# Kernel tuning notes

Measured on AMD Instinct MI355X. Metric: run time of the kernel, lower is better.

The kernel has to match this reference:

```python
import jax, jax.numpy as jnp
import numpy as np

N = 8192
F_IN = 256
F_OUT = 64
NEG_SLOPE = 0.01


def setup_inputs() -> dict:
    key = jax.random.key(0)
    k1, k2, k3, k4 = jax.random.split(key, 4)
    h = jax.random.normal(k1, (N, F_IN), dtype=jnp.float32)
    adj = jax.random.randint(k2, (N, N), 0, 2).astype(jnp.float32)
    # xavier_uniform-scaled params
    W = jax.random.uniform(k3, (F_IN, F_OUT), jnp.float32, -1.0, 1.0) * np.sqrt(6.0 / (F_IN + F_OUT)).astype(np.float32)
    a = jax.random.uniform(k4, (2 * F_OUT, 1), jnp.float32, -1.0, 1.0) * np.sqrt(6.0 / (2 * F_OUT + 1)).astype(np.float32)
    return {"h": h, "adj": adj, "W": W, "a": a, "rel": 0}


def reference(h, adj, W, a, rel):
    # Wh: [N, F']
    Wh = h @ W
    # Decompose additive score: e_ij = LeakyReLU(a1.Wh_i + a2.Wh_j)
    # (equivalent to cat([Wh_i, Wh_j]) @ a, without the [N,N,2F'] tensor)
    a1 = a[:F_OUT, 0]
    a2 = a[F_OUT:, 0]
    f1 = Wh @ a1  # [N]
    f2 = Wh @ a2  # [N]
    e = jax.nn.leaky_relu(f1[:, None] + f2[None, :], NEG_SLOPE)  # [N, N]
    e = jnp.where(adj > 0, e, -jnp.inf)
    attention = jax.nn.softmax(e, axis=1)  # dropout is identity at eval time
    h_prime = attention @ Wh  # [N, F']
    return h_prime, attention
```

## Files before the change

### kernel.cpp

```cpp
#include <hip/hip_runtime.h>
#include <hip/hip_bf16.h>

#define N 8192
#define FIN 256
#define FOUT 64
#define NEG_SLOPE 0.01f
#define CHUNK 256
#define NCHUNK (N / CHUNK)
#define ROWS_B 8

typedef float f32x4 __attribute__((ext_vector_type(4)));
typedef __bf16 bf16x8 __attribute__((ext_vector_type(8)));
typedef unsigned long long ull;

__device__ __forceinline__ float lk(float x) { return x >= 0.f ? x : NEG_SLOPE * x; }

__global__ __launch_bounds__(256) void gat_k1(const float* __restrict__ h,
                                              const float* __restrict__ W,
                                              const float* __restrict__ a,
                                              unsigned short* __restrict__ WhB,
                                              float* __restrict__ f1,
                                              float* __restrict__ f2) {
  __shared__ float Ws[FIN * FOUT];
  const int t = threadIdx.x;
  const int lane = t & 63;
  const int w = t >> 6;
  const size_t row0 = (size_t)blockIdx.x * 16;

  for (int i = t; i < FIN * FOUT / 4; i += 256)
    ((f32x4*)Ws)[i] = ((const f32x4*)W)[i];
  __syncthreads();

  const float* h0 = h + row0 * FIN;
  float acc[4] = {0.f, 0.f, 0.f, 0.f};
  #pragma unroll 4
  for (int c4 = 0; c4 < FIN; c4 += 4) {
    const f32x4 hv0 = *(const f32x4*)(h0 + (w + 0)  * FIN + c4);
    const f32x4 hv1 = *(const f32x4*)(h0 + (w + 4)  * FIN + c4);
    const f32x4 hv2 = *(const f32x4*)(h0 + (w + 8)  * FIN + c4);
    const f32x4 hv3 = *(const f32x4*)(h0 + (w + 12) * FIN + c4);
    #pragma unroll
    for (int j = 0; j < 4; ++j) {
      const float wv = Ws[(c4 + j) * FOUT + lane];
      acc[0] = fmaf(hv0[j], wv, acc[0]);
      acc[1] = fmaf(hv1[j], wv, acc[1]);
      acc[2] = fmaf(hv2[j], wv, acc[2]);
      acc[3] = fmaf(hv3[j], wv, acc[3]);
    }
  }

  const float a1k = a[lane];
  const float a2k = a[FOUT + lane];
  #pragma unroll
  for (int i = 0; i < 4; ++i) {
    const size_t row = row0 + (w + 4 * i);
    WhB[(((row >> 3) * 64) + lane) * 8 + (row & 7)] =
        __builtin_bit_cast(unsigned short, __float2bfloat16(acc[i]));
    float p1 = acc[i] * a1k, p2 = acc[i] * a2k;
    #pragma unroll
    for (int off = 32; off; off >>= 1) {
      p1 += __shfl_down(p1, off);
      p2 += __shfl_down(p2, off);
    }
    if (lane == 0) { f1[row] = p1; f2[row] = p2; }
  }
}

__global__ __launch_bounds__(512) void gat_k2a(const float* __restrict__ adj,
                                               const float* __restrict__ f1g,
                                               const float* __restrict__ f2g,
                                               ull* __restrict__ mskg,
                                               float* __restrict__ izg) {
  __shared__ float f2s[N];
  const int t = threadIdx.x;
  const int lane = t & 63;
  const int w = t >> 6;
  for (int i = t; i < N / 4; i += 512)
    ((f32x4*)f2s)[i] = ((const f32x4*)f2g)[i];
  __syncthreads();

  const int row = blockIdx.x * 8 + w;
  const float f1r = f1g[row];
  const f32x4* arow = (const f32x4*)(adj + (size_t)row * N);
  ull* mrow = mskg + (size_t)row * (NCHUNK * 4);

  float s = 0.f;
  #pragma unroll 8
  for (int c = 0; c < NCHUNK; ++c) {
    const f32x4 v = arow[c * 64 + lane];
    const f32x4 f = *(const f32x4*)&f2s[c * CHUNK + lane * 4];
    const ull b0 = __ballot(v.x > 0.f);
    const ull b1 = __ballot(v.y > 0.f);
    const ull b2 = __ballot(v.z > 0.f);
    const ull b3 = __ballot(v.w > 0.f);
    const ull bb = lane == 0 ? b0 : lane == 1 ? b1 : lane == 2 ? b2 : b3;
    if (lane < 4) mrow[c * 4 + lane] = bb;
    s += (v.x > 0.f) ? __expf(lk(f1r + f.x)) : 0.f;
    s += (v.y > 0.f) ? __expf(lk(f1r + f.y)) : 0.f;
    s += (v.z > 0.f) ? __expf(lk(f1r + f.z)) : 0.f;
    s += (v.w > 0.f) ? __expf(lk(f1r + f.w)) : 0.f;
  }
  #pragma unroll
  for (int off = 32; off; off >>= 1) s += __shfl_xor(s, off);
  if (lane == 0) izg[row] = 1.f / s;
}

__global__ __launch_bounds__(512) void gat_k2b(const ull* __restrict__ mskg,
                                               const float* __restrict__ f1g,
                                               const float* __restrict__ f2g,
                                               const float* __restrict__ izg,
                                               const unsigned short* __restrict__ WhB,
                                               float* __restrict__ att,
                                               float* __restrict__ hp) {
  __shared__ ull msk[ROWS_B * NCHUNK * 4];
  __shared__ __align__(16) unsigned char attb[16 * CHUNK * 2];
  __shared__ float red[4][64][4];
  __shared__ float f1s[ROWS_B], izs[ROWS_B];

  const int t = threadIdx.x;
  const int lane = t & 63;
  const int w = t >> 6;
  const size_t row0 = (size_t)blockIdx.x * ROWS_B;

  for (int i = t; i < ROWS_B * NCHUNK * 4; i += 512)
    msk[i] = mskg[row0 * (NCHUNK * 4) + i];
  for (int i = t; i < 16 * CHUNK * 2 / 4; i += 512)
    ((unsigned int*)attb)[i] = 0u;
  if (t < ROWS_B) { f1s[t] = f1g[row0 + t]; izs[t] = izg[row0 + t]; }
  __syncthreads();

  const int ks = w >> 2, nt = w & 3;
  const int r = w;
  const float f1r = f1s[r], z = izs[r];
  f32x4 acc = {0.f, 0.f, 0.f, 0.f};

  for (int c = 0; c < NCHUNK; ++c) {
    const f32x4 f = *(const f32x4*)&f2g[c * CHUNK + lane * 4];
    const ull b0 = msk[r * (NCHUNK * 4) + c * 4 + 0];
    const ull b1 = msk[r * (NCHUNK * 4) + c * 4 + 1];
    const ull b2 = msk[r * (NCHUNK * 4) + c * 4 + 2];
    const ull b3 = msk[r * (NCHUNK * 4) + c * 4 + 3];
    f32x4 p;
    p.x = ((b0 >> lane) & 1ull) ? __expf(lk(f1r + f.x)) * z : 0.f;
    p.y = ((b1 >> lane) & 1ull) ? __expf(lk(f1r + f.y)) * z : 0.f;
    p.z = ((b2 >> lane) & 1ull) ? __expf(lk(f1r + f.z)) * z : 0.f;
    p.w = ((b3 >> lane) & 1ull) ? __expf(lk(f1r + f.w)) * z : 0.f;
    __builtin_nontemporal_store(p, (f32x4*)(att + (row0 + r) * (size_t)N + c * CHUNK + lane * 4));
    const ull pk =
        (ull)__builtin_bit_cast(unsigned short, __float2bfloat16(p.x)) |
        ((ull)__builtin_bit_cast(unsigned short, __float2bfloat16(p.y)) << 16) |
        ((ull)__builtin_bit_cast(unsigned short, __float2bfloat16(p.z)) << 32) |
        ((ull)__builtin_bit_cast(unsigned short, __float2bfloat16(p.w)) << 48);
    int byte = r * (CHUNK * 2) + lane * 8;
    byte ^= (r & 7) << 4;
    *(ull*)(attb + byte) = pk;
    __syncthreads();

    #pragma unroll
    for (int s = 0; s < 4; ++s) {
      const int mf = ks * 4 + s;
      const int arow_ = lane & 15;
      int ab = arow_ * (CHUNK * 2) + mf * 64 + (lane >> 4) * 16;
      ab ^= (arow_ & 7) << 4;
      const bf16x8 afrag = *(const bf16x8*)(attb + ab);
      const int kg = c * 32 + mf * 4 + (lane >> 4);
      const bf16x8 bfrag = *(const bf16x8*)(WhB + ((size_t)kg * 64 + nt * 16 + (lane & 15)) * 8);
      acc = __builtin_amdgcn_mfma_f32_16x16x32_bf16(afrag, bfrag, acc, 0, 0, 0);
    }
    __syncthreads();
  }

  if (ks == 1) *(f32x4*)&red[nt][lane][0] = acc;
  __syncthreads();
  if (ks == 0) {
    const f32x4 o = acc + *(const f32x4*)&red[nt][lane][0];
    const int col = nt * 16 + (lane & 15);
    const int rbase = (lane >> 4) * 4;
    if (rbase < ROWS_B) {
      #pragma unroll
      for (int q = 0; q < 4; ++q)
        hp[(row0 + rbase + q) * FOUT + col] = o[q];
    }
  }
}

extern "C" void kernel_launch(void* const* d_in, const int* in_sizes, int n_in,
                              void* d_out, int out_size, void* d_ws, size_t ws_size,
                              hipStream_t stream) {
  const float* h   = (const float*)d_in[0];
  const float* adj = (const float*)d_in[1];
  const float* W   = (const float*)d_in[2];
  const float* a   = (const float*)d_in[3];

  float* hp  = (float*)d_out;
  float* att = hp + (size_t)N * FOUT;

  unsigned short* WhB = (unsigned short*)d_ws;
  float* f1 = (float*)((char*)d_ws + (size_t)N * FOUT * 2);
  float* f2 = f1 + N;
  float* iz = f2 + N;
  ull*   msk = (ull*)(iz + N);

  gat_k1 <<<N / 16, 256, 0, stream>>>(h, W, a, WhB, f1, f2);
  gat_k2a<<<N / 8, 512, 0, stream>>>(adj, f1, f2, msk, iz);
  gat_k2b<<<N / ROWS_B, 512, 0, stream>>>(msk, f1, f2, iz, WhB, att, hp);
}
```

Measured before the change: 534.5 us.

## Widen attention-matmul tile to 32 rows with double-buffered LDS and no split-K

The second-pass kernel now handles 32 rows per block instead of 8. Each wave computes four rows of attention and a full 16x16 MFMA output tile over the whole K chunk, so the split-K reduction and the wasted half-empty MFMA rows go away. The LDS attention buffer is double-buffered, which removes one barrier per chunk. Mask bits are read straight from global memory instead of being staged in LDS. The first-pass kernel also stops staging f2 in LDS and uses nontemporal loads for adj. The risk is fewer blocks (256) with fewer waves to hide latency, plus more global mask loads per wave.

```diff
diff --git a/kernel.cpp b/kernel.cpp
--- a/kernel.cpp
+++ b/kernel.cpp
@@ -7,7 +7,8 @@
 #define NEG_SLOPE 0.01f
 #define CHUNK 256
 #define NCHUNK (N / CHUNK)
-#define ROWS_B 8
+#define RB 32
+#define MWORDS (NCHUNK * 4)
 
 typedef float f32x4 __attribute__((ext_vector_type(4)));
 typedef __bf16 bf16x8 __attribute__((ext_vector_type(8)));
@@ -71,24 +72,19 @@
                                                const float* __restrict__ f2g,
                                                ull* __restrict__ mskg,
                                                float* __restrict__ izg) {
-  __shared__ float f2s[N];
   const int t = threadIdx.x;
   const int lane = t & 63;
   const int w = t >> 6;
-  for (int i = t; i < N / 4; i += 512)
-    ((f32x4*)f2s)[i] = ((const f32x4*)f2g)[i];
-  __syncthreads();
-
   const int row = blockIdx.x * 8 + w;
   const float f1r = f1g[row];
   const f32x4* arow = (const f32x4*)(adj + (size_t)row * N);
-  ull* mrow = mskg + (size_t)row * (NCHUNK * 4);
+  ull* mrow = mskg + (size_t)row * MWORDS;
 
   float s = 0.f;
-  #pragma unroll 8
+  #pragma unroll 4
   for (int c = 0; c < NCHUNK; ++c) {
-    const f32x4 v = arow[c * 64 + lane];
-    const f32x4 f = *(const f32x4*)&f2s[c * CHUNK + lane * 4];
+    const f32x4 v = __builtin_nontemporal_load(arow + c * 64 + lane);
+    const f32x4 f = *(const f32x4*)&f2g[c * CHUNK + lane * 4];
     const ull b0 = __ballot(v.x > 0.f);
     const ull b1 = __ballot(v.y > 0.f);
     const ull b2 = __ballot(v.z > 0.f);
@@ -112,76 +108,64 @@
                                                const unsigned short* __restrict__ WhB,
                                                float* __restrict__ att,
                                                float* __restrict__ hp) {
-  __shared__ ull msk[ROWS_B * NCHUNK * 4];
-  __shared__ __align__(16) unsigned char attb[16 * CHUNK * 2];
-  __shared__ float red[4][64][4];
-  __shared__ float f1s[ROWS_B], izs[ROWS_B];
-
+  __shared__ __align__(16) unsigned char attb[2][RB * CHUNK * 2];
   const int t = threadIdx.x;
   const int lane = t & 63;
   const int w = t >> 6;
-  const size_t row0 = (size_t)blockIdx.x * ROWS_B;
+  const int mt = w >> 2, nt = w & 3;
+  const size_t row0 = (size_t)blockIdx.x * RB;
 
-  for (int i = t; i < ROWS_B * NCHUNK * 4; i += 512)
-    msk[i] = mskg[row0 * (NCHUNK * 4) + i];
-  for (int i = t; i < 16 * CHUNK * 2 / 4; i += 512)
-    ((unsigned int*)attb)[i] = 0u;
-  if (t < ROWS_B) { f1s[t] = f1g[row0 + t]; izs[t] = izg[row0 + t]; }
-  __syncthreads();
+  float f1r_[4], z_[4];
+  #pragma unroll
+  for (int rr = 0; rr < 4; ++rr) {
+    f1r_[rr] = f1g[row0 + 4 * w + rr];
+    z_[rr]   = izg[row0 + 4 * w + rr];
+  }
 
-  const int ks = w >> 2, nt = w & 3;
-  const int r = w;
-  const float f1r = f1s[r], z = izs[r];
   f32x4 acc = {0.f, 0.f, 0.f, 0.f};
 
+  #pragma unroll 2
   for (int c = 0; c < NCHUNK; ++c) {
+    unsigned char* ab = attb[c & 1];
     const f32x4 f = *(const f32x4*)&f2g[c * CHUNK + lane * 4];
-    const ull b0 = msk[r * (NCHUNK * 4) + c * 4 + 0];
-    const ull b1 = msk[r * (NCHUNK * 4) + c * 4 + 1];
-    const ull b2 = msk[r * (NCHUNK * 4) + c * 4 + 2];
-    const ull b3 = msk[r * (NCHUNK * 4) + c * 4 + 3];
-    f32x4 p;
-    p.x = ((b0 >> lane) & 1ull) ? __expf(lk(f1r + f.x)) * z : 0.f;
-    p.y = ((b1 >> lane) & 1ull) ? __expf(lk(f1r + f.y)) * z : 0.f;
-    p.z = ((b2 >> lane) & 1ull) ? __expf(lk(f1r + f.z)) * z : 0.f;
-    p.w = ((b3 >> lane) & 1ull) ? __expf(lk(f1r + f.w)) * z : 0.f;
-    __builtin_nontemporal_store(p, (f32x4*)(att + (row0 + r) * (size_t)N + c * CHUNK + lane * 4));
-    const ull pk =
-        (ull)__builtin_bit_cast(unsigned short, __float2bfloat16(p.x)) |
-        ((ull)__builtin_bit_cast(unsigned short, __float2bfloat16(p.y)) << 16) |
-        ((ull)__builtin_bit_cast(unsigned short, __float2bfloat16(p.z)) << 32) |
-        ((ull)__builtin_bit_cast(unsigned short, __float2bfloat16(p.w)) << 48);
-    int byte = r * (CHUNK * 2) + lane * 8;
-    byte ^= (r & 7) << 4;
-    *(ull*)(attb + byte) = pk;
+    #pragma unroll
+    for (int rr = 0; rr < 4; ++rr) {
+      const int r = 4 * w + rr;
+      const ull* mrow = mskg + (row0 + r) * (size_t)MWORDS + c * 4;
+      const ull b0 = mrow[0], b1 = mrow[1], b2 = mrow[2], b3 = mrow[3];
+      f32x4 p;
+      p.x = ((b0 >> lane) & 1ull) ? __expf(lk(f1r_[rr] + f.x)) * z_[rr] : 0.f;
+      p.y = ((b1 >> lane) & 1ull) ? __expf(lk(f1r_[rr] + f.y)) * z_[rr] : 0.f;
+      p.z = ((b2 >> lane) & 1ull) ? __expf(lk(f1r_[rr] + f.z)) * z_[rr] : 0.f;
+      p.w = ((b3 >> lane) & 1ull) ? __expf(lk(f1r_[rr] + f.w)) * z_[rr] : 0.f;
+      __builtin_nontemporal_store(p, (f32x4*)(att + (row0 + r) * (size_t)N + c * CHUNK + lane * 4));
+      const ull pk =
+          (ull)__builtin_bit_cast(unsigned short, __float2bfloat16(p.x)) |
+          ((ull)__builtin_bit_cast(unsigned short, __float2bfloat16(p.y)) << 16) |
+          ((ull)__builtin_bit_cast(unsigned short, __float2bfloat16(p.z)) << 32) |
+          ((ull)__builtin_bit_cast(unsigned short, __float2bfloat16(p.w)) << 48);
+      int byte = r * (CHUNK * 2) + lane * 8;
+      byte ^= (r & 7) << 4;
+      *(ull*)(ab + byte) = pk;
+    }
     __syncthreads();
-
     #pragma unroll
-    for (int s = 0; s < 4; ++s) {
-      const int mf = ks * 4 + s;
-      const int arow_ = lane & 15;
-      int ab = arow_ * (CHUNK * 2) + mf * 64 + (lane >> 4) * 16;
-      ab ^= (arow_ & 7) << 4;
-      const bf16x8 afrag = *(const bf16x8*)(attb + ab);
-      const int kg = c * 32 + mf * 4 + (lane >> 4);
+    for (int s = 0; s < 8; ++s) {
+      const int arow_ = mt * 16 + (lane & 15);
+      int off = arow_ * (CHUNK * 2) + s * 64 + (lane >> 4) * 16;
+      off ^= (arow_ & 7) << 4;
+      const bf16x8 afrag = *(const bf16x8*)(ab + off);
+      const int kg = c * 32 + s * 4 + (lane >> 4);
       const bf16x8 bfrag = *(const bf16x8*)(WhB + ((size_t)kg * 64 + nt * 16 + (lane & 15)) * 8);
       acc = __builtin_amdgcn_mfma_f32_16x16x32_bf16(afrag, bfrag, acc, 0, 0, 0);
     }
-    __syncthreads();
   }
 
-  if (ks == 1) *(f32x4*)&red[nt][lane][0] = acc;
-  __syncthreads();
-  if (ks == 0) {
-    const f32x4 o = acc + *(const f32x4*)&red[nt][lane][0];
-    const int col = nt * 16 + (lane & 15);
-    const int rbase = (lane >> 4) * 4;
-    if (rbase < ROWS_B) {
-      #pragma unroll
-      for (int q = 0; q < 4; ++q)
-        hp[(row0 + rbase + q) * FOUT + col] = o[q];
-    }
-  }
+  const int col = nt * 16 + (lane & 15);
+  const int rbase = mt * 16 + (lane >> 4) * 4;
+  #pragma unroll
+  for (int q = 0; q < 4; ++q)
+    hp[(row0 + rbase + q) * FOUT + col] = acc[q];
 }
 
 extern "C" void kernel_launch(void* const* d_in, const int* in_sizes, int n_in,
@@ -203,5 +187,5 @@
 
   gat_k1 <<<N / 16, 256, 0, stream>>>(h, W, a, WhB, f1, f2);
   gat_k2a<<<N / 8, 512, 0, stream>>>(adj, f1, f2, msk, iz);
-  gat_k2b<<<N / ROWS_B, 512, 0, stream>>>(msk, f1, f2, iz, WhB, att, hp);
+  gat_k2b<<<N / RB, 512, 0, stream>>>(msk, f1, f2, iz, WhB, att, hp);
 }
```

After: 521.2 us. -2.5%, faster.
